# Performance work log

Hardware: AMD Instinct MI355X
Metric: run time of the kernel (lower is better)

Reference implementation:

```python
import math
import jax, jax.numpy as jnp
import numpy as np

EMBED_DIM = 512
NUM_HEADS = 8
EDGE_VOC = 16
EDGE_PAD = 0
L, B = 512, 16


def setup_inputs() -> dict:
    key = jax.random.key(0)
    ks = jax.random.split(key, 8)
    x = jax.random.normal(ks[0], (L, B, EMBED_DIM), dtype=jnp.float32)
    edge = jax.random.randint(ks[1], (B, L, L), 0, EDGE_VOC, dtype=jnp.int32)
    key_padding_mask = jnp.zeros((B, L), dtype=bool)
    # causal additive mask, as from nn.Transformer.generate_square_subsequent_mask
    attn_mask = jnp.where(jnp.triu(jnp.ones((L, L), bool), k=1), -jnp.inf, 0.0).astype(jnp.float32)
    s = 1.0 / math.sqrt(EMBED_DIM)
    in_proj_w = jax.random.uniform(ks[2], (3 * EMBED_DIM, EMBED_DIM), jnp.float32, -s, s)
    in_proj_b = jnp.zeros((3 * EMBED_DIM,), jnp.float32)
    out_proj_w = jax.random.uniform(ks[3], (EMBED_DIM, EMBED_DIM), jnp.float32, -s, s)
    out_proj_b = jnp.zeros((EMBED_DIM,), jnp.float32)
    edge_emb = jax.random.normal(ks[4], (EDGE_VOC, NUM_HEADS), dtype=jnp.float32)
    edge_emb = edge_emb.at[EDGE_PAD].set(0.0)  # padding_idx row zeroed
    return {"x": x, "edge": edge, "key_padding_mask": key_padding_mask,
            "attn_mask": attn_mask, "in_proj_w": in_proj_w, "in_proj_b": in_proj_b,
            "out_proj_w": out_proj_w, "out_proj_b": out_proj_b, "edge_emb": edge_emb}


def reference(x, edge, key_padding_mask, attn_mask,
              in_proj_w, in_proj_b, out_proj_w, out_proj_b, edge_emb):
    length, bsz, embed_dim = x.shape
    H = edge_emb.shape[1]
    hd = embed_dim // H
    qkv = x @ in_proj_w.T + in_proj_b                       # (L, B, 3E)
    q, k, v = jnp.split(qkv, 3, axis=-1)
    # (L, B*H, hd) -> (B*H, L, hd)
    q = q.reshape(length, bsz * H, hd).transpose(1, 0, 2)
    k = k.reshape(length, bsz * H, hd).transpose(1, 0, 2)
    v = v.reshape(length, bsz * H, hd).transpose(1, 0, 2)
    # combine attn_mask with key padding
    mask = attn_mask[None]                                   # (1, L, L)
    kpm = jnp.broadcast_to(key_padding_mask[:, None, None, :],
                           (bsz, H, 1, length)).reshape(bsz * H, 1, length)
    mask = jnp.where(kpm, -jnp.inf, mask)                    # (B*H, 1/L, L)
    # edge bias: (B, L, L, H) -> (B*H, L, L)
    ebias = edge_emb[edge].transpose(0, 3, 1, 2).reshape(bsz * H, length, length)
    q = q / math.sqrt(hd)
    scores = jnp.einsum('bqd,bkd->bqk', q, k) + mask + ebias
    attn = jax.nn.softmax(scores, axis=-1)
    out = jnp.einsum('bqk,bkd->bqd', attn, v)                # (B*H, L, hd)
    out = out.transpose(1, 0, 2).reshape(length, bsz, embed_dim)
    return out @ out_proj_w.T + out_proj_b
```

## Files before the change

### kernel.cpp

```cpp
#include <hip/hip_runtime.h>
#include <hip/hip_bf16.h>


typedef __attribute__((ext_vector_type(8))) short bf16x8;
typedef __attribute__((ext_vector_type(4))) float f32x4;
typedef __attribute__((ext_vector_type(4))) int i32x4;

#define LOG2E 1.44269504088896340736f

__device__ inline void gll16(const void* g, const void* l) {
  __builtin_amdgcn_global_load_lds(
      (const __attribute__((address_space(1))) unsigned int*)g,
      (__attribute__((address_space(3))) unsigned int*)l, 16, 0, 0);
}

__device__ inline short f2bf(float x) {
  __hip_bfloat16 t = __float2bfloat16(x);
  return *reinterpret_cast<short*>(&t);
}

__device__ inline void cstore(__hip_bfloat16* C, size_t idx, float v) {
  C[idx] = __float2bfloat16(v);
}
__device__ inline void cstore(float* C, size_t idx, float v) { C[idx] = v; }

__global__ void cvt3(const float* __restrict__ x, const float* __restrict__ w1,
                     const float* __restrict__ w2, __hip_bfloat16* __restrict__ xb,
                     __hip_bfloat16* __restrict__ w1b,
                     __hip_bfloat16* __restrict__ w2b) {
  const int blk = blockIdx.x;
  const float* src;
  __hip_bfloat16* dst;
  int off;
  if (blk < 2048)      { src = x;  dst = xb;  off = blk; }
  else if (blk < 2432) { src = w1; dst = w1b; off = blk - 2048; }
  else                 { src = w2; dst = w2b; off = blk - 2432; }
  const int i = (off * 256 + threadIdx.x) * 8;
  const float4 a = *(const float4*)(src + i);
  const float4 b = *(const float4*)(src + i + 4);
  bf16x8 r;
  r[0] = f2bf(a.x); r[1] = f2bf(a.y); r[2] = f2bf(a.z); r[3] = f2bf(a.w);
  r[4] = f2bf(b.x); r[5] = f2bf(b.y); r[6] = f2bf(b.z); r[7] = f2bf(b.w);
  *(bf16x8*)(dst + i) = r;
}

template <int MT, int RB, typename TC>
__global__ __launch_bounds__(256, RB) void gemm_bt(
    const __hip_bfloat16* __restrict__ A,
    const __hip_bfloat16* __restrict__ W,
    const float* __restrict__ bias,
    TC* __restrict__ C, int N, int K) {
  constexpr int MI = MT / 32;
  __shared__ short As[MT * 32];
  __shared__ short Ws[128 * 32];
  const int tid = threadIdx.x;
  const int wave = tid >> 6, lane = tid & 63;
  const int c = lane & 15, quad = lane >> 4;
  const int nb = N >> 7;
  const int bx = blockIdx.x % nb, by = blockIdx.x / nb;
  const int m0 = by * MT, n0 = bx << 7;
  const int wm = wave >> 1, wn = wave & 1;

  f32x4 acc[MI][4] = {};
  const int ar = lane >> 2;
  const int ak = (lane & 3) * 8;

  for (int k0 = 0; k0 < K; k0 += 32) {
    __syncthreads();
#pragma unroll
    for (int i = 0; i < MT / 64; i++) {
      const int r0 = i * 64 + wave * 16;
      gll16(A + (size_t)(m0 + r0 + ar) * K + k0 + ak, &As[r0 * 32]);
    }
#pragma unroll
    for (int i = 0; i < 2; i++) {
      const int r0 = i * 64 + wave * 16;
      gll16(W + (size_t)(n0 + r0 + ar) * K + k0 + ak, &Ws[r0 * 32]);
    }
    __syncthreads();
    bf16x8 af[MI], bfr[4];
#pragma unroll
    for (int i = 0; i < MI; i++)
      af[i] = *(const bf16x8*)&As[(wm * (MT / 2) + i * 16 + c) * 32 + quad * 8];
#pragma unroll
    for (int j = 0; j < 4; j++)
      bfr[j] = *(const bf16x8*)&Ws[(wn * 64 + j * 16 + c) * 32 + quad * 8];
#pragma unroll
    for (int i = 0; i < MI; i++)
#pragma unroll
      for (int j = 0; j < 4; j++)
        acc[i][j] = __builtin_amdgcn_mfma_f32_16x16x32_bf16(af[i], bfr[j],
                                                            acc[i][j], 0, 0, 0);
  }
#pragma unroll
  for (int j = 0; j < 4; j++) {
    const int col = n0 + wn * 64 + j * 16 + c;
    const float bv = bias[col];
#pragma unroll
    for (int i = 0; i < MI; i++) {
      const int row = m0 + wm * (MT / 2) + i * 16 + quad * 4;
#pragma unroll
      for (int r = 0; r < 4; r++)
        cstore(C, (size_t)(row + r) * N + col, acc[i][j][r] + bv);
    }
  }
}

__global__ __launch_bounds__(256, 4) void attn_kernel(
    const __hip_bfloat16* __restrict__ qkv,
    const int* __restrict__ edge,
    const float* __restrict__ edge_emb,
    __hip_bfloat16* __restrict__ attn_out) {
  __shared__ short Ks[64 * 72];
  __shared__ short Vt[64 * 72];
  __shared__ short Ps[4][16 * 72];
  __shared__ float eeS[16];

  const int tid = threadIdx.x;
  const int wave = tid >> 6, lane = tid & 63;
  const int c = lane & 15, quad = lane >> 4;
  const int i = blockIdx.x;
  constexpr int pi[8] = {0, 7, 1, 6, 2, 5, 3, 4};
  const int xcd = i & 7;
  const int j = i >> 3;
  const int qb = pi[j & 7];
  const int h = (j >> 3) & 7;
  const int b = xcd + ((j >> 6) << 3);
  const int colq = h * 64;

  if (tid < 16) eeS[tid] = (edge_emb[tid * 8 + h] - 16.0f) * LOG2E;

  const int q_g = (qb << 6) + wave * 16 + c;
  bf16x8 qf0, qf1;
  {
    const __hip_bfloat16* qp_ = qkv + (size_t)(q_g * 16 + b) * 1536 + colq;
    qf0 = *(const bf16x8*)(qp_ + quad * 8);
    qf1 = *(const bf16x8*)(qp_ + 32 + quad * 8);
  }
  float lsum = 0.f;
  f32x4 o[4] = {};
  const int* erow = edge + ((size_t)(b * 512 + q_g)) * 512;

  const int r2 = tid >> 3;
  const int cc = (tid & 7) * 8;
  const int kcol0 = ((r2 << 1) & 7) | (((r2 >> 2) ^ (cc >> 3)) << 3);
  const size_t sbase0 = (size_t)((r2 * 2) * 16 + b) * 1536 + colq + cc;
  bf16x8 kreg[2], vreg[2];
  kreg[0] = *(const bf16x8*)(qkv + sbase0 + 512);
  vreg[0] = *(const bf16x8*)(qkv + sbase0 + 1024);
  kreg[1] = *(const bf16x8*)(qkv + sbase0 + 24576 + 512);
  vreg[1] = *(const bf16x8*)(qkv + sbase0 + 24576 + 1024);

  __syncthreads();

  const int nkt = qb + 1;
  for (int kt = 0; kt < nkt; kt++) {
    const int k0 = kt << 6;
    if (kt) __syncthreads();
    *(bf16x8*)&Ks[(r2 * 2) * 72 + cc] = kreg[0];
    *(bf16x8*)&Ks[(r2 * 2 + 1) * 72 + cc] = kreg[1];
#pragma unroll
    for (int j2 = 0; j2 < 8; j2++) {
      short2 p;
      p.x = vreg[0][j2];
      p.y = vreg[1][j2];
      *(short2*)&Vt[(cc + j2) * 72 + kcol0] = p;
    }
    if (kt + 1 < nkt) {
      const size_t nb_ = sbase0 + (size_t)(kt + 1) * 64 * 24576;
      kreg[0] = *(const bf16x8*)(qkv + nb_ + 512);
      vreg[0] = *(const bf16x8*)(qkv + nb_ + 1024);
      kreg[1] = *(const bf16x8*)(qkv + nb_ + 24576 + 512);
      vreg[1] = *(const bf16x8*)(qkv + nb_ + 24576 + 1024);
    }
    i32x4 e4[4];
#pragma unroll
    for (int mt = 0; mt < 4; mt++)
      e4[mt] = *(const i32x4*)(erow + k0 + mt * 16 + quad * 4);
    __syncthreads();

    f32x4 st[4];
#pragma unroll
    for (int mt = 0; mt < 4; mt++) {
      const bf16x8 ka = *(const bf16x8*)&Ks[(mt * 16 + c) * 72 + quad * 8];
      const bf16x8 kb = *(const bf16x8*)&Ks[(mt * 16 + c) * 72 + 32 + quad * 8];
      f32x4 z = {0.f, 0.f, 0.f, 0.f};
      z = __builtin_amdgcn_mfma_f32_16x16x32_bf16(ka, qf0, z, 0, 0, 0);
      st[mt] = __builtin_amdgcn_mfma_f32_16x16x32_bf16(kb, qf1, z, 0, 0, 0);
    }
    float rsum = 0.0f;
#pragma unroll
    for (int mt = 0; mt < 4; mt++) {
      short4 pk;
#pragma unroll
      for (int r = 0; r < 4; r++) {
        const int key = k0 + mt * 16 + quad * 4 + r;
        const float p = (key <= q_g)
            ? exp2f(fmaf(st[mt][r], 0.125f * LOG2E, eeS[e4[mt][r] & 15]))
            : 0.0f;
        rsum += p;
        ((short*)&pk)[r] = f2bf(p);
      }
      *(short4*)&Ps[wave][c * 72 + mt * 16 + quad * 4] = pk;
    }
    lsum += rsum;
    const bf16x8 pa0 = *(const bf16x8*)&Ps[wave][c * 72 + quad * 8];
    const bf16x8 pa1 = *(const bf16x8*)&Ps[wave][c * 72 + 32 + quad * 8];
#pragma unroll
    for (int nt = 0; nt < 4; nt++) {
      const int n = nt * 16 + c;
      const bf16x8 vb0 = *(const bf16x8*)&Vt[n * 72 + ((quad ^ (n >> 3)) << 3)];
      const bf16x8 vb1 =
          *(const bf16x8*)&Vt[n * 72 + (((4 + quad) ^ (n >> 3)) << 3)];
      o[nt] = __builtin_amdgcn_mfma_f32_16x16x32_bf16(pa0, vb0, o[nt], 0, 0, 0);
      o[nt] = __builtin_amdgcn_mfma_f32_16x16x32_bf16(pa1, vb1, o[nt], 0, 0, 0);
    }
  }

  float l = lsum;
  l += __shfl_xor(l, 16);
  l += __shfl_xor(l, 32);
  float lr[4];
#pragma unroll
  for (int r = 0; r < 4; r++) lr[r] = __shfl(l, quad * 4 + r, 16);
  const int qrow0 = (qb << 6) + wave * 16 + quad * 4;
#pragma unroll
  for (int nt = 0; nt < 4; nt++)
#pragma unroll
    for (int r = 0; r < 4; r++)
      attn_out[(size_t)((qrow0 + r) * 16 + b) * 512 + colq + nt * 16 + c] =
          __float2bfloat16(o[nt][r] / lr[r]);
}

extern "C" void kernel_launch(void* const* d_in, const int* in_sizes, int n_in,
                              void* d_out, int out_size, void* d_ws, size_t ws_size,
                              hipStream_t stream) {
  const float* x    = (const float*)d_in[0];
  const int* edge   = (const int*)d_in[1];
  const float* ipw  = (const float*)d_in[4];
  const float* ipb  = (const float*)d_in[5];
  const float* opw  = (const float*)d_in[6];
  const float* opb  = (const float*)d_in[7];
  const float* eemb = (const float*)d_in[8];
  float* out = (float*)d_out;

  __hip_bfloat16* qkv  = (__hip_bfloat16*)d_ws;
  __hip_bfloat16* attn = qkv + (size_t)8192 * 1536;
  __hip_bfloat16* xb   = attn + (size_t)8192 * 512;
  __hip_bfloat16* w1b  = xb + (size_t)8192 * 512;
  __hip_bfloat16* w2b  = w1b + (size_t)1536 * 512;

  cvt3<<<2560, 256, 0, stream>>>(x, ipw, opw, xb, w1b, w2b);
  gemm_bt<128, 3, __hip_bfloat16>
      <<<768, 256, 0, stream>>>(xb, w1b, ipb, qkv, 1536, 512);
  attn_kernel<<<1024, 256, 0, stream>>>(qkv, edge, eemb, attn);
  gemm_bt<64, 2, float>
      <<<512, 256, 0, stream>>>(attn, w2b, opb, out, 512, 512);
}
```

Before: 155.6 us.

## Restructure attention: double-buffered prefetch, fused scale, batch-major QKV, causal skipping

```diff
diff --git a/kernel.cpp b/kernel.cpp
--- a/kernel.cpp
+++ b/kernel.cpp
@@ -7,6 +7,7 @@
 typedef __attribute__((ext_vector_type(4))) int i32x4;
 
 #define LOG2E 1.44269504088896340736f
+#define QK_SCALE 0.18033688011112042f
 
 __device__ inline void gll16(const void* g, const void* l) {
   __builtin_amdgcn_global_load_lds(
@@ -44,7 +45,7 @@
   *(bf16x8*)(dst + i) = r;
 }
 
-template <int MT, int RB, typename TC>
+template <int MT, int RB, typename TC, bool QS = false, bool BROW = false>
 __global__ __launch_bounds__(256, RB) void gemm_bt(
     const __hip_bfloat16* __restrict__ A,
     const __hip_bfloat16* __restrict__ W,
@@ -100,8 +101,15 @@
     for (int i = 0; i < MI; i++) {
       const int row = m0 + wm * (MT / 2) + i * 16 + quad * 4;
 #pragma unroll
-      for (int r = 0; r < 4; r++)
-        cstore(C, (size_t)(row + r) * N + col, acc[i][j][r] + bv);
+      for (int r = 0; r < 4; r++) {
+        float v = acc[i][j][r] + bv;
+        if constexpr (QS) {
+          if (col < 512) v *= QK_SCALE;
+        }
+        int orow = row + r;
+        if constexpr (BROW) orow = ((orow & 15) << 9) | (orow >> 4);
+        cstore(C, (size_t)orow * N + col, v);
+      }
     }
   }
 }
@@ -123,99 +131,143 @@
   constexpr int pi[8] = {0, 7, 1, 6, 2, 5, 3, 4};
   const int xcd = i & 7;
   const int j = i >> 3;
-  const int qb = pi[j & 7];
+  const int qb = pi[(j + (j >> 5)) & 7];
   const int h = (j >> 3) & 7;
   const int b = xcd + ((j >> 6) << 3);
   const int colq = h * 64;
+  const int nkt = qb + 1;
 
   if (tid < 16) eeS[tid] = (edge_emb[tid * 8 + h] - 16.0f) * LOG2E;
 
   const int q_g = (qb << 6) + wave * 16 + c;
-  bf16x8 qf0, qf1;
-  {
-    const __hip_bfloat16* qp_ = qkv + (size_t)(q_g * 16 + b) * 1536 + colq;
-    qf0 = *(const bf16x8*)(qp_ + quad * 8);
-    qf1 = *(const bf16x8*)(qp_ + 32 + quad * 8);
-  }
-  float lsum = 0.f;
-  f32x4 o[4] = {};
   const int* erow = edge + ((size_t)(b * 512 + q_g)) * 512;
 
   const int r2 = tid >> 3;
   const int cc = (tid & 7) * 8;
   const int kcol0 = ((r2 << 1) & 7) | (((r2 >> 2) ^ (cc >> 3)) << 3);
-  const size_t sbase0 = (size_t)((r2 * 2) * 16 + b) * 1536 + colq + cc;
-  bf16x8 kreg[2], vreg[2];
-  kreg[0] = *(const bf16x8*)(qkv + sbase0 + 512);
-  vreg[0] = *(const bf16x8*)(qkv + sbase0 + 1024);
-  kreg[1] = *(const bf16x8*)(qkv + sbase0 + 24576 + 512);
-  vreg[1] = *(const bf16x8*)(qkv + sbase0 + 24576 + 1024);
+  const size_t sbase0 = (size_t)(b * 512 + r2 * 2) * 1536 + colq + cc;
+
+  i32x4 eA[4], eB[4];
+  bf16x8 krA[2], vrA[2], krB[2], vrB[2];
+#pragma unroll
+  for (int mt = 0; mt < 4; mt++)
+    eA[mt] = *(const i32x4*)(erow + mt * 16 + quad * 4);
+  krA[0] = *(const bf16x8*)(qkv + sbase0 + 512);
+  vrA[0] = *(const bf16x8*)(qkv + sbase0 + 1024);
+  krA[1] = *(const bf16x8*)(qkv + sbase0 + 1536 + 512);
+  vrA[1] = *(const bf16x8*)(qkv + sbase0 + 1536 + 1024);
+  if (nkt > 1) {
+#pragma unroll
+    for (int mt = 0; mt < 4; mt++)
+      eB[mt] = *(const i32x4*)(erow + 64 + mt * 16 + quad * 4);
+    const size_t b1 = sbase0 + 64 * 1536;
+    krB[0] = *(const bf16x8*)(qkv + b1 + 512);
+    vrB[0] = *(const bf16x8*)(qkv + b1 + 1024);
+    krB[1] = *(const bf16x8*)(qkv + b1 + 1536 + 512);
+    vrB[1] = *(const bf16x8*)(qkv + b1 + 1536 + 1024);
+  }
+
+  bf16x8 qf0, qf1;
+  {
+    const __hip_bfloat16* qp_ = qkv + (size_t)(b * 512 + q_g) * 1536 + colq;
+    qf0 = *(const bf16x8*)(qp_ + quad * 8);
+    qf1 = *(const bf16x8*)(qp_ + 32 + quad * 8);
+  }
+  float lsum = 0.f;
+  f32x4 o[4] = {};
 
   __syncthreads();
 
-  const int nkt = qb + 1;
-  for (int kt = 0; kt < nkt; kt++) {
-    const int k0 = kt << 6;
-    if (kt) __syncthreads();
-    *(bf16x8*)&Ks[(r2 * 2) * 72 + cc] = kreg[0];
-    *(bf16x8*)&Ks[(r2 * 2 + 1) * 72 + cc] = kreg[1];
-#pragma unroll
-    for (int j2 = 0; j2 < 8; j2++) {
-      short2 p;
-      p.x = vreg[0][j2];
-      p.y = vreg[1][j2];
-      *(short2*)&Vt[(cc + j2) * 72 + kcol0] = p;
-    }
-    if (kt + 1 < nkt) {
-      const size_t nb_ = sbase0 + (size_t)(kt + 1) * 64 * 24576;
-      kreg[0] = *(const bf16x8*)(qkv + nb_ + 512);
-      vreg[0] = *(const bf16x8*)(qkv + nb_ + 1024);
-      kreg[1] = *(const bf16x8*)(qkv + nb_ + 24576 + 512);
-      vreg[1] = *(const bf16x8*)(qkv + nb_ + 24576 + 1024);
-    }
-    i32x4 e4[4];
-#pragma unroll
-    for (int mt = 0; mt < 4; mt++)
-      e4[mt] = *(const i32x4*)(erow + k0 + mt * 16 + quad * 4);
-    __syncthreads();
-
-    f32x4 st[4];
-#pragma unroll
-    for (int mt = 0; mt < 4; mt++) {
-      const bf16x8 ka = *(const bf16x8*)&Ks[(mt * 16 + c) * 72 + quad * 8];
-      const bf16x8 kb = *(const bf16x8*)&Ks[(mt * 16 + c) * 72 + 32 + quad * 8];
-      f32x4 z = {0.f, 0.f, 0.f, 0.f};
-      z = __builtin_amdgcn_mfma_f32_16x16x32_bf16(ka, qf0, z, 0, 0, 0);
-      st[mt] = __builtin_amdgcn_mfma_f32_16x16x32_bf16(kb, qf1, z, 0, 0, 0);
-    }
-    float rsum = 0.0f;
-#pragma unroll
-    for (int mt = 0; mt < 4; mt++) {
-      short4 pk;
-#pragma unroll
-      for (int r = 0; r < 4; r++) {
-        const int key = k0 + mt * 16 + quad * 4 + r;
-        const float p = (key <= q_g)
-            ? exp2f(fmaf(st[mt][r], 0.125f * LOG2E, eeS[e4[mt][r] & 15]))
-            : 0.0f;
-        rsum += p;
-        ((short*)&pk)[r] = f2bf(p);
-      }
-      *(short4*)&Ps[wave][c * 72 + mt * 16 + quad * 4] = pk;
-    }
-    lsum += rsum;
-    const bf16x8 pa0 = *(const bf16x8*)&Ps[wave][c * 72 + quad * 8];
-    const bf16x8 pa1 = *(const bf16x8*)&Ps[wave][c * 72 + 32 + quad * 8];
-#pragma unroll
-    for (int nt = 0; nt < 4; nt++) {
-      const int n = nt * 16 + c;
-      const bf16x8 vb0 = *(const bf16x8*)&Vt[n * 72 + ((quad ^ (n >> 3)) << 3)];
-      const bf16x8 vb1 =
-          *(const bf16x8*)&Vt[n * 72 + (((4 + quad) ^ (n >> 3)) << 3)];
-      o[nt] = __builtin_amdgcn_mfma_f32_16x16x32_bf16(pa0, vb0, o[nt], 0, 0, 0);
-      o[nt] = __builtin_amdgcn_mfma_f32_16x16x32_bf16(pa1, vb1, o[nt], 0, 0, 0);
-    }
-  }
+  int kt = 0;
+#define ATTN_STEP(E, KR, VR)                                                   \
+  {                                                                            \
+    const int k0 = kt << 6;                                                    \
+    const bool last = (kt == qb);                                              \
+    const int mtmax = last ? (wave + 1) : 4;                                   \
+    if (kt) __syncthreads();                                                   \
+    *(bf16x8*)&Ks[(r2 * 2) * 72 + cc] = KR[0];                                 \
+    *(bf16x8*)&Ks[(r2 * 2 + 1) * 72 + cc] = KR[1];                             \
+    _Pragma("unroll") for (int j2 = 0; j2 < 8; j2++) {                         \
+      short2 p;                                                                \
+      p.x = VR[0][j2];                                                         \
+      p.y = VR[1][j2];                                                         \
+      *(short2*)&Vt[(cc + j2) * 72 + kcol0] = p;                               \
+    }                                                                          \
+    if (kt + 2 < nkt) {                                                        \
+      const size_t nb_ = sbase0 + (size_t)(kt + 2) * 64 * 1536;                \
+      KR[0] = *(const bf16x8*)(qkv + nb_ + 512);                               \
+      VR[0] = *(const bf16x8*)(qkv + nb_ + 1024);                              \
+      KR[1] = *(const bf16x8*)(qkv + nb_ + 1536 + 512);                        \
+      VR[1] = *(const bf16x8*)(qkv + nb_ + 1536 + 1024);                       \
+    }                                                                          \
+    __syncthreads();                                                           \
+    f32x4 st[4];                                                               \
+    __builtin_amdgcn_s_setprio(1);                                             \
+    _Pragma("unroll") for (int mt = 0; mt < 4; mt++) {                         \
+      if (mt >= mtmax) continue;                                               \
+      f32x4 z;                                                                 \
+      _Pragma("unroll") for (int r = 0; r < 4; r++) z[r] = eeS[E[mt][r]];      \
+      const bf16x8 ka = *(const bf16x8*)&Ks[(mt * 16 + c) * 72 + quad * 8];    \
+      const bf16x8 kb =                                                        \
+          *(const bf16x8*)&Ks[(mt * 16 + c) * 72 + 32 + quad * 8];             \
+      z = __builtin_amdgcn_mfma_f32_16x16x32_bf16(ka, qf0, z, 0, 0, 0);        \
+      st[mt] = __builtin_amdgcn_mfma_f32_16x16x32_bf16(kb, qf1, z, 0, 0, 0);   \
+    }                                                                          \
+    __builtin_amdgcn_s_setprio(0);                                             \
+    if (kt + 2 < nkt) {                                                        \
+      const int kn = (kt + 2) << 6;                                            \
+      _Pragma("unroll") for (int mt = 0; mt < 4; mt++)                         \
+          E[mt] = *(const i32x4*)(erow + kn + mt * 16 + quad * 4);             \
+    }                                                                          \
+    float rs[4] = {0.f, 0.f, 0.f, 0.f};                                        \
+    _Pragma("unroll") for (int mt = 0; mt < 4; mt++) {                         \
+      short4 pk = {0, 0, 0, 0};                                                \
+      if (mt < mtmax) {                                                        \
+        if (last && mt == wave) {                                              \
+          _Pragma("unroll") for (int r = 0; r < 4; r++) {                      \
+            const float p = (quad * 4 + r <= c) ? exp2f(st[mt][r]) : 0.0f;     \
+            rs[r] += p;                                                        \
+            ((short*)&pk)[r] = f2bf(p);                                        \
+          }                                                                    \
+        } else {                                                               \
+          _Pragma("unroll") for (int r = 0; r < 4; r++) {                      \
+            const float p = exp2f(st[mt][r]);                                  \
+            rs[r] += p;                                                        \
+            ((short*)&pk)[r] = f2bf(p);                                        \
+          }                                                                    \
+        }                                                                      \
+      }                                                                        \
+      *(short4*)&Ps[wave][c * 72 + mt * 16 + quad * 4] = pk;                   \
+    }                                                                          \
+    lsum += (rs[0] + rs[1]) + (rs[2] + rs[3]);                                 \
+    const bool skip_hi = last && (wave < 2);                                   \
+    const bf16x8 pa0 = *(const bf16x8*)&Ps[wave][c * 72 + quad * 8];           \
+    bf16x8 pa1;                                                                \
+    if (!skip_hi) pa1 = *(const bf16x8*)&Ps[wave][c * 72 + 32 + quad * 8];     \
+    __builtin_amdgcn_s_setprio(1);                                             \
+    _Pragma("unroll") for (int nt = 0; nt < 4; nt++) {                         \
+      const int n = nt * 16 + c;                                               \
+      const bf16x8 vb0 =                                                       \
+          *(const bf16x8*)&Vt[n * 72 + ((quad ^ (n >> 3)) << 3)];              \
+      o[nt] = __builtin_amdgcn_mfma_f32_16x16x32_bf16(pa0, vb0, o[nt], 0, 0,   \
+                                                      0);                      \
+      if (!skip_hi) {                                                          \
+        const bf16x8 vb1 =                                                     \
+            *(const bf16x8*)&Vt[n * 72 + (((4 + quad) ^ (n >> 3)) << 3)];      \
+        o[nt] = __builtin_amdgcn_mfma_f32_16x16x32_bf16(pa1, vb1, o[nt], 0, 0, \
+                                                        0);                    \
+      }                                                                        \
+    }                                                                          \
+    __builtin_amdgcn_s_setprio(0);                                             \
+  }
+
+  while (true) {
+    ATTN_STEP(eA, krA, vrA);
+    if (++kt == nkt) break;
+    ATTN_STEP(eB, krB, vrB);
+    if (++kt == nkt) break;
+  }
+#undef ATTN_STEP
 
   float l = lsum;
   l += __shfl_xor(l, 16);
@@ -251,7 +303,7 @@
   __hip_bfloat16* w2b  = w1b + (size_t)1536 * 512;
 
   cvt3<<<2560, 256, 0, stream>>>(x, ipw, opw, xb, w1b, w2b);
-  gemm_bt<128, 3, __hip_bfloat16>
+  gemm_bt<128, 3, __hip_bfloat16, true, true>
       <<<768, 256, 0, stream>>>(xb, w1b, ipb, qkv, 1536, 512);
   attn_kernel<<<1024, 256, 0, stream>>>(qkv, edge, eemb, attn);
   gemm_bt<64, 2, float>
```

After: 178.6 us. 1.15x slower.
